# Kernel optimization log

Hardware: AMD Instinct MI355X
Metric: run time of the kernel (lower is better)

## Reference

```python
import jax, jax.numpy as jnp
import numpy as np

B, K, L, D, H = 8, 64, 4096, 1024, 16
HD = D // H
SCALE = HD ** -0.5


def setup_inputs() -> dict:
    key = jax.random.key(0)
    ks = jax.random.split(key, 7)
    return {
        "query": jax.random.normal(ks[0], (B, K, D), jnp.float32),
        "key": jax.random.normal(ks[1], (B, L, D), jnp.float32),
        "value": jax.random.normal(ks[2], (B, L, D), jnp.float32),
        "Wq": jax.random.normal(ks[3], (D, D), jnp.float32) * (D ** -0.5),
        "Wk": jax.random.normal(ks[4], (D, D), jnp.float32) * (D ** -0.5),
        "Wv": jax.random.normal(ks[5], (D, D), jnp.float32) * (D ** -0.5),
        "Wo": jax.random.normal(ks[6], (D, D), jnp.float32) * (D ** -0.5),
        "bo": jnp.zeros((D,), jnp.float32),
    }


def reference(query, key, value, Wq, Wk, Wv, Wo, bo):
    # torch Linear: y = x @ W.T; split heads -> [B,H,len,HD]
    q = jnp.einsum('bkd,ed->bke', query, Wq).reshape(B, K, H, HD).transpose(0, 2, 1, 3)
    k = jnp.einsum('bld,ed->ble', key, Wk).reshape(B, L, H, HD).transpose(0, 2, 1, 3)
    v = jnp.einsum('bld,ed->ble', value, Wv).reshape(B, L, H, HD).transpose(0, 2, 1, 3)
    dots = jnp.einsum('bhkc,bhlc->bhkl', q, k) * SCALE  # [B,H,K,L]
    attn = jax.nn.softmax(dots, axis=-2)               # softmax over query (slot) dim
    attn = attn / (attn.sum(axis=-1, keepdims=True) + 1e-8)  # renormalize over keys
    out = jnp.einsum('bhkl,bhlc->bhkc', attn, v)       # [B,H,K,HD]
    out = out.transpose(0, 2, 1, 3).reshape(B, K, D)
    out = jnp.einsum('bkd,ed->bke', out, Wo) + bo
    return out, attn
```

## Files before the change

### kernel.cpp

```cpp
#include <hip/hip_runtime.h>
#include <hip/hip_bf16.h>

#define B_   8
#define KS_  64
#define L_   4096
#define D_   1024
#define H_   16
#define HD_  64
#define SCALE_ 0.125f

typedef __attribute__((ext_vector_type(8))) short short8;
typedef __attribute__((ext_vector_type(8))) unsigned short ushort8;
typedef __attribute__((ext_vector_type(4))) unsigned short ushort4v;
typedef __attribute__((ext_vector_type(4))) float f32x4;

__device__ __forceinline__ unsigned short f2b(float f) {
  union { float f; unsigned u; } v; v.f = f;
  unsigned r = v.u + 0x7fffu + ((v.u >> 16) & 1u);
  return (unsigned short)(r >> 16);
}

typedef const __attribute__((address_space(1))) void gas_void;
typedef __attribute__((address_space(3))) void las_void;
__device__ __forceinline__ void gl2lds16(const void* g, void* l) {
  __builtin_amdgcn_global_load_lds((gas_void*)g, (las_void*)l, 16, 0, 0);
}

__global__ __launch_bounds__(256) void wcvt(const float* __restrict__ wq,
                                            const float* __restrict__ wk,
                                            const float* __restrict__ wv,
                                            const float* __restrict__ wo,
                                            unsigned short* __restrict__ out) {
  int i = blockIdx.x * 256 + threadIdx.x;
  int seg = i >> 18;
  int off = (i & 0x3ffff) << 2;
  const float* src = (seg == 0) ? wq : (seg == 1) ? wk : (seg == 2) ? wv : wo;
  f32x4 v = *(const f32x4*)(src + off);
  ushort4v o;
#pragma unroll
  for (int j = 0; j < 4; ++j) o[j] = f2b(v[j]);
  *(ushort4v*)(out + ((size_t)seg << 20) + off) = o;
}

__global__ __launch_bounds__(256) void cvt_qkv(const float* __restrict__ q,
                                               const float* __restrict__ k,
                                               const float* __restrict__ v,
                                               unsigned short* __restrict__ qb,
                                               unsigned short* __restrict__ kb,
                                               unsigned short* __restrict__ vb) {
  const int Q4 = 131072, K4 = 8388608;
  const int total = Q4 + 2 * K4;
  for (int i = blockIdx.x * 256 + threadIdx.x; i < total; i += gridDim.x * 256) {
    const float* src; unsigned short* dst; int off;
    if (i < Q4)            { src = q; dst = qb; off = i; }
    else if (i < Q4 + K4)  { src = k; dst = kb; off = i - Q4; }
    else                   { src = v; dst = vb; off = i - Q4 - K4; }
    f32x4 x = *(const f32x4*)(src + (size_t)off * 4);
    ushort4v o;
#pragma unroll
    for (int j = 0; j < 4; ++j) o[j] = f2b(x[j]);
    *(ushort4v*)(dst + (size_t)off * 4) = o;
  }
}

template <bool OUT_F32B>
__global__ __launch_bounds__(256) void gemm_bf16(const unsigned short* __restrict__ A,
                                                 const unsigned short* __restrict__ W,
                                                 void* __restrict__ Cp,
                                                 const float* __restrict__ bias) {
  __shared__ __align__(16) char smem[34816];
  const int tid = threadIdx.x, lane = tid & 63, wv = tid >> 6;
  const int g = lane >> 4, c15 = lane & 15;
  const int wm = wv >> 1, wn = wv & 1;

  const int nwg = gridDim.x;
  const int swz = (blockIdx.x & 7) * (nwg >> 3) + (blockIdx.x >> 3);
  const long m0 = (long)(swz >> 3) * 128;
  const int  n0 = (swz & 7) * 128;

  const int srow = lane >> 2, scol = (lane & 3) * 8;
  const unsigned short* a_src = A + (m0 + srow) * 1024 + scol;
  const unsigned short* b_src = W + (long)(n0 + srow) * 1024 + scol;

  f32x4 acc[4][4] = {};

  auto stage = [&](int buf, int kt) {
    unsigned short* al = (unsigned short*)(smem + buf * 8192);
    unsigned short* bl = (unsigned short*)(smem + 16384 + buf * 8192);
#pragma unroll
    for (int q = 0; q < 2; ++q) {
      const int rbase = q * 64 + wv * 16;
      gl2lds16(a_src + (long)rbase * 1024 + kt * 32, al + rbase * 32);
      gl2lds16(b_src + (long)rbase * 1024 + kt * 32, bl + rbase * 32);
    }
  };

  stage(0, 0);
  __syncthreads();

  int cur = 0;
  for (int kt = 0; kt < 32; ++kt) {
    if (kt + 1 < 32) stage(cur ^ 1, kt + 1);
    const unsigned short* al = (const unsigned short*)(smem + cur * 8192);
    const unsigned short* bl = (const unsigned short*)(smem + 16384 + cur * 8192);
    short8 af[4];
#pragma unroll
    for (int m = 0; m < 4; ++m)
      af[m] = *(const short8*)&al[(wm * 64 + m * 16 + c15) * 32 + g * 8];
#pragma unroll
    for (int n = 0; n < 4; ++n) {
      short8 b8 = *(const short8*)&bl[(wn * 64 + n * 16 + c15) * 32 + g * 8];
#pragma unroll
      for (int m = 0; m < 4; ++m)
        acc[m][n] = __builtin_amdgcn_mfma_f32_16x16x32_bf16(af[m], b8, acc[m][n], 0, 0, 0);
    }
    __syncthreads();
    cur ^= 1;
  }

  if constexpr (OUT_F32B) {
    float* Cf = (float*)Cp;
#pragma unroll
    for (int m = 0; m < 4; ++m)
#pragma unroll
      for (int n = 0; n < 4; ++n)
#pragma unroll
        for (int r = 0; r < 4; ++r) {
          long row = m0 + wm * 64 + m * 16 + g * 4 + r;
          int  col = n0 + wn * 64 + n * 16 + c15;
          Cf[row * 1024 + col] = acc[m][n][r] + bias[col];
        }
  } else {
    unsigned short* c_lds = (unsigned short*)smem;
#pragma unroll
    for (int m = 0; m < 4; ++m)
#pragma unroll
      for (int n = 0; n < 4; ++n)
#pragma unroll
        for (int r = 0; r < 4; ++r)
          c_lds[(wm * 64 + m * 16 + g * 4 + r) * 132 + wn * 64 + n * 16 + c15] =
              f2b(acc[m][n][r]);
    __syncthreads();
    unsigned short* Cb = (unsigned short*)Cp;
    const int row = tid >> 1, half = tid & 1;
    unsigned short*       dst = Cb + (m0 + row) * 1024 + n0 + half * 64;
    const unsigned short* sl  = &c_lds[row * 132 + half * 64];
#pragma unroll
    for (int i = 0; i < 8; ++i)
      *(ushort8*)(dst + i * 8) = *(const ushort8*)(sl + i * 8);
  }
}

__global__ __launch_bounds__(512) void attn_pass1(const unsigned short* __restrict__ q_b,
                                                  const unsigned short* __restrict__ k_b,
                                                  float* __restrict__ rs_part) {
  __shared__ unsigned short q_lds[64][72];
  __shared__ unsigned short k_lds[128][72];
  __shared__ float rs_lds[8][64];
  const int bh = blockIdx.x >> 2, ch = blockIdx.x & 3;
  const int b = bh >> 4, h = bh & 15;
  const int tid = threadIdx.x;
  const int w = tid >> 6, lane = tid & 63;
  const int g = lane >> 4, c15 = lane & 15;

  {
    int slot = tid >> 3, cc = (tid & 7) * 8;
    *(ushort8*)&q_lds[slot][cc] =
        *(const ushort8*)(q_b + (long)(b * 64 + slot) * 1024 + h * 64 + cc);
  }

  float rs[4][4] = {};
  const long kbase = (long)b * L_ * D_ + h * 64;
  const int  sl = tid >> 2, sc = (tid & 3) * 16;

  for (int it = ch * 8; it < ch * 8 + 8; ++it) {
    const int l0 = it * 128;
    ushort8 k0 = *(const ushort8*)(k_b + kbase + (long)(l0 + sl) * 1024 + sc);
    ushort8 k1 = *(const ushort8*)(k_b + kbase + (long)(l0 + sl) * 1024 + sc + 8);
    __syncthreads();
    *(ushort8*)&k_lds[sl][sc]     = k0;
    *(ushort8*)&k_lds[sl][sc + 8] = k1;
    __syncthreads();

    f32x4 s[4] = {};
#pragma unroll
    for (int ks = 0; ks < 2; ++ks) {
      short8 bf = *(const short8*)&k_lds[w * 16 + c15][ks * 32 + g * 8];
#pragma unroll
      for (int m = 0; m < 4; ++m) {
        short8 af = *(const short8*)&q_lds[m * 16 + c15][ks * 32 + g * 8];
        s[m] = __builtin_amdgcn_mfma_f32_16x16x32_bf16(af, bf, s[m], 0, 0, 0);
      }
    }
    float mx = -1e30f;
#pragma unroll
    for (int m = 0; m < 4; ++m)
#pragma unroll
      for (int r = 0; r < 4; ++r) mx = fmaxf(mx, s[m][r]);
    mx = fmaxf(mx, __shfl_xor(mx, 16));
    mx = fmaxf(mx, __shfl_xor(mx, 32));
    float sum = 0.f, p[4][4];
#pragma unroll
    for (int m = 0; m < 4; ++m)
#pragma unroll
      for (int r = 0; r < 4; ++r) { p[m][r] = __expf((s[m][r] - mx) * SCALE_); sum += p[m][r]; }
    sum += __shfl_xor(sum, 16);
    sum += __shfl_xor(sum, 32);
    float rinv = 1.0f / sum;
#pragma unroll
    for (int m = 0; m < 4; ++m)
#pragma unroll
      for (int r = 0; r < 4; ++r) rs[m][r] += p[m][r] * rinv;
  }
#pragma unroll
  for (int m = 0; m < 4; ++m)
#pragma unroll
    for (int r = 0; r < 4; ++r) {
      float v = rs[m][r];
      v += __shfl_xor(v, 1); v += __shfl_xor(v, 2);
      v += __shfl_xor(v, 4); v += __shfl_xor(v, 8);
      if (c15 == 0) rs_lds[w][m * 16 + g * 4 + r] = v;
    }
  __syncthreads();
  if (tid < 64) {
    float t = 0.f;
#pragma unroll
    for (int w2 = 0; w2 < 8; ++w2) t += rs_lds[w2][tid];
    rs_part[(bh * 4 + ch) * 64 + tid] = t;
  }
}

__global__ __launch_bounds__(512) void attn_pass2(const unsigned short* __restrict__ q_b,
                                                  const unsigned short* __restrict__ k_b,
                                                  const unsigned short* __restrict__ v_b,
                                                  const float* __restrict__ rs_part,
                                                  float* __restrict__ attn,
                                                  float* __restrict__ op_part) {
  __shared__ unsigned short q_lds[64][72];
  __shared__ unsigned short k_lds[128][72];
  __shared__ unsigned short vt_lds[64][136];
  __shared__ unsigned short pt_lds[64][136];
  const int bh = blockIdx.x >> 2, ch = blockIdx.x & 3;
  const int b = bh >> 4, h = bh & 15;
  const int tid = threadIdx.x;
  const int w = tid >> 6, lane = tid & 63;
  const int g = lane >> 4, c15 = lane & 15;

  {
    int slot = tid >> 3, cc = (tid & 7) * 8;
    *(ushort8*)&q_lds[slot][cc] =
        *(const ushort8*)(q_b + (long)(b * 64 + slot) * 1024 + h * 64 + cc);
  }

  float inv_r[4][4];
#pragma unroll
  for (int m = 0; m < 4; ++m)
#pragma unroll
    for (int r = 0; r < 4; ++r) {
      int slot = m * 16 + g * 4 + r;
      float s = 0.f;
#pragma unroll
      for (int c = 0; c < 4; ++c) s += rs_part[(bh * 4 + c) * 64 + slot];
      inv_r[m][r] = 1.0f / (s + 1e-8f);
    }

  f32x4 oacc[2] = {};
  const int m_pv = w >> 1, n_pv0 = (w & 1) * 2;
  float* attn_base = attn + (long)bh * KS_ * L_;
  const long base_bld = (long)b * L_ * D_ + h * 64;
  const int  sl = tid >> 2, sc = (tid & 3) * 16;

  for (int it = ch * 8; it < ch * 8 + 8; ++it) {
    const int l0 = it * 128;
    ushort8 k0 = *(const ushort8*)(k_b + base_bld + (long)(l0 + sl) * 1024 + sc);
    ushort8 k1 = *(const ushort8*)(k_b + base_bld + (long)(l0 + sl) * 1024 + sc + 8);
    ushort8 v0 = *(const ushort8*)(v_b + base_bld + (long)(l0 + sl) * 1024 + sc);
    ushort8 v1 = *(const ushort8*)(v_b + base_bld + (long)(l0 + sl) * 1024 + sc + 8);
    __syncthreads();
    *(ushort8*)&k_lds[sl][sc]     = k0;
    *(ushort8*)&k_lds[sl][sc + 8] = k1;
#pragma unroll
    for (int j = 0; j < 8; ++j) {
      vt_lds[sc + j][sl]     = v0[j];
      vt_lds[sc + 8 + j][sl] = v1[j];
    }
    __syncthreads();

    f32x4 s[4] = {};
#pragma unroll
    for (int ks = 0; ks < 2; ++ks) {
      short8 bf = *(const short8*)&k_lds[w * 16 + c15][ks * 32 + g * 8];
#pragma unroll
      for (int m = 0; m < 4; ++m) {
        short8 af = *(const short8*)&q_lds[m * 16 + c15][ks * 32 + g * 8];
        s[m] = __builtin_amdgcn_mfma_f32_16x16x32_bf16(af, bf, s[m], 0, 0, 0);
      }
    }
    float mx = -1e30f;
#pragma unroll
    for (int m = 0; m < 4; ++m)
#pragma unroll
      for (int r = 0; r < 4; ++r) mx = fmaxf(mx, s[m][r]);
    mx = fmaxf(mx, __shfl_xor(mx, 16));
    mx = fmaxf(mx, __shfl_xor(mx, 32));
    float sum = 0.f, p[4][4];
#pragma unroll
    for (int m = 0; m < 4; ++m)
#pragma unroll
      for (int r = 0; r < 4; ++r) { p[m][r] = __expf((s[m][r] - mx) * SCALE_); sum += p[m][r]; }
    sum += __shfl_xor(sum, 16);
    sum += __shfl_xor(sum, 32);
    float rinv = 1.0f / sum;

    const int lloc = w * 16 + c15;
#pragma unroll
    for (int m = 0; m < 4; ++m)
#pragma unroll
      for (int r = 0; r < 4; ++r) {
        float ps = p[m][r] * rinv * inv_r[m][r];
        attn_base[(long)(m * 16 + g * 4 + r) * L_ + l0 + lloc] = ps;
        pt_lds[m * 16 + g * 4 + r][lloc] = f2b(ps);
      }
    __syncthreads();

#pragma unroll
    for (int ks = 0; ks < 4; ++ks) {
      short8 pa = *(const short8*)&pt_lds[m_pv * 16 + c15][ks * 32 + g * 8];
#pragma unroll
      for (int n2 = 0; n2 < 2; ++n2) {
        short8 vb = *(const short8*)&vt_lds[(n_pv0 + n2) * 16 + c15][ks * 32 + g * 8];
        oacc[n2] = __builtin_amdgcn_mfma_f32_16x16x32_bf16(pa, vb, oacc[n2], 0, 0, 0);
      }
    }
  }

#pragma unroll
  for (int n2 = 0; n2 < 2; ++n2)
#pragma unroll
    for (int r = 0; r < 4; ++r) {
      int slot = m_pv * 16 + g * 4 + r;
      int c    = (n_pv0 + n2) * 16 + c15;
      op_part[((long)(bh * 4 + ch) * 64 + slot) * 64 + c] = oacc[n2][r];
    }
}

__global__ __launch_bounds__(256) void oh_red(const float* __restrict__ op_part,
                                              unsigned short* __restrict__ oh) {
  int i = blockIdx.x * 256 + threadIdx.x;
  int c = i & 63, slot = (i >> 6) & 63, bh = i >> 12;
  float s = 0.f;
#pragma unroll
  for (int ch = 0; ch < 4; ++ch)
    s += op_part[((long)(bh * 4 + ch) * 64 + slot) * 64 + c];
  int b = bh >> 4, h = bh & 15;
  oh[(long)(b * 64 + slot) * 1024 + h * 64 + c] = f2b(s);
}

extern "C" void kernel_launch(void* const* d_in, const int* in_sizes, int n_in,
                              void* d_out, int out_size, void* d_ws, size_t ws_size,
                              hipStream_t stream) {
  (void)in_sizes; (void)n_in; (void)out_size; (void)ws_size;
  const float* query = (const float*)d_in[0];
  const float* key   = (const float*)d_in[1];
  const float* value = (const float*)d_in[2];
  const float* Wq    = (const float*)d_in[3];
  const float* Wk    = (const float*)d_in[4];
  const float* Wv    = (const float*)d_in[5];
  const float* Wo    = (const float*)d_in[6];
  const float* bo    = (const float*)d_in[7];

  char* ws = (char*)d_ws;
  unsigned short* w_all   = (unsigned short*)ws;
  unsigned short* wq_b    = w_all;
  unsigned short* wk_b    = w_all + (1u << 20);
  unsigned short* wv_b    = w_all + (2u << 20);
  unsigned short* wo_b    = w_all + (3u << 20);
  unsigned short* qin_b   = (unsigned short*)(ws + ((size_t)8  << 20));
  unsigned short* q_b     = (unsigned short*)(ws + ((size_t)9  << 20));
  unsigned short* oh_b    = (unsigned short*)(ws + ((size_t)10 << 20));
  float*          rs_part = (float*)         (ws + ((size_t)11 << 20));
  float*          op_part = (float*)         (ws + ((size_t)12 << 20));
  unsigned short* k_b     = (unsigned short*)(ws + ((size_t)20 << 20));
  unsigned short* v_b     = (unsigned short*)(ws + ((size_t)84 << 20));

  float* out  = (float*)d_out;
  float* attn = out + (size_t)B_ * KS_ * D_;

  unsigned short* kin_b = (unsigned short*)attn;
  unsigned short* vin_b = (unsigned short*)attn + ((size_t)32 << 20);

  wcvt<<<4096, 256, 0, stream>>>(Wq, Wk, Wv, Wo, w_all);
  cvt_qkv<<<2048, 256, 0, stream>>>(query, key, value, qin_b, kin_b, vin_b);

  gemm_bf16<false><<<32,   256, 0, stream>>>(qin_b, wq_b, q_b, nullptr);
  gemm_bf16<false><<<2048, 256, 0, stream>>>(kin_b, wk_b, k_b, nullptr);
  gemm_bf16<false><<<2048, 256, 0, stream>>>(vin_b, wv_b, v_b, nullptr);

  attn_pass1<<<512, 512, 0, stream>>>(q_b, k_b, rs_part);
  attn_pass2<<<512, 512, 0, stream>>>(q_b, k_b, v_b, rs_part, attn, op_part);
  oh_red<<<2048, 256, 0, stream>>>(op_part, oh_b);

  gemm_bf16<true><<<32, 256, 0, stream>>>(oh_b, wo_b, out, bo);
}
```

Measured before the change: 420.9 us.

## Add 256x256-tile double-buffered bf16 GEMM for K and V projections

Adds a new 512-thread GEMM kernel with 256x256 output tiles, 128KB LDS double buffering via direct global-to-LDS loads, XOR-swizzled LDS layout, and interleaved stage/MFMA phases with priority boosts. It replaces the 128x128 gemm for the large K and V projections (32768x1024x1024 each). Larger tiles raise arithmetic intensity and cut global reloads. The cost is lower occupancy and a fragile hand-written waitcnt/barrier schedule.

New measurement: 391.5 us. 1.08x faster.

```diff
diff --git a/kernel.cpp b/kernel.cpp
--- a/kernel.cpp
+++ b/kernel.cpp
@@ -24,6 +24,15 @@
 typedef __attribute__((address_space(3))) void las_void;
 __device__ __forceinline__ void gl2lds16(const void* g, void* l) {
   __builtin_amdgcn_global_load_lds((gas_void*)g, (las_void*)l, 16, 0, 0);
+}
+
+__device__ __forceinline__ void bar() {
+  asm volatile("" ::: "memory");
+  __builtin_amdgcn_s_barrier();
+  asm volatile("" ::: "memory");
+}
+__device__ __forceinline__ void vm4() {
+  asm volatile("s_waitcnt vmcnt(4)" ::: "memory");
 }
 
 __global__ __launch_bounds__(256) void wcvt(const float* __restrict__ wq,
@@ -63,6 +72,97 @@
   }
 }
 
+__global__ __launch_bounds__(512, 2) void gemm256(const unsigned short* __restrict__ A,
+                                                  const unsigned short* __restrict__ W,
+                                                  unsigned short* __restrict__ C) {
+  __shared__ __align__(16) char smem[131072];
+  const int tid = threadIdx.x, lane = tid & 63, w = tid >> 6;
+  const int g = lane >> 4, c15 = lane & 15;
+  const int wm = w >> 2, wn = w & 3;
+
+  const int swz = (blockIdx.x & 7) * 64 + (blockIdx.x >> 3);
+  const long m0 = (long)(swz >> 2) * 256;
+  const int  n0 = (swz & 2 * 2 - 1) * 256;
+
+  const int srow = w * 16 + (lane >> 2);
+  const int cswz = (lane & 3) ^ ((lane >> 2) & 3);
+  const unsigned short* a_sr = A + (m0 + srow) * 1024 + cswz * 8;
+  const unsigned short* b_sr = W + (long)(n0 + srow) * 1024 + cswz * 8;
+  const int rswz = (g ^ (c15 & 3)) << 4;
+  const int aoff = (wm * 128 + c15) * 64 + rswz;
+  const int boff = 65536 + (wn * 64 + c15) * 64 + rswz;
+
+  f32x4 acc[8][4] = {};
+  short8 af[8], bf[2];
+
+  auto STAGE_A = [&](int d, int kh, int tk) {
+    char* dst = smem + d * 32768 + kh * 16384 + w * 1024;
+    const unsigned short* src = a_sr + tk * 64 + kh * 32;
+    gl2lds16(src,          dst);
+    gl2lds16(src + 131072, dst + 8192);
+  };
+  auto STAGE_B = [&](int d, int kh, int tk) {
+    char* dst = smem + 65536 + d * 32768 + kh * 16384 + w * 1024;
+    const unsigned short* src = b_sr + tk * 64 + kh * 32;
+    gl2lds16(src,          dst);
+    gl2lds16(src + 131072, dst + 8192);
+  };
+  auto LDA = [&](int d, int ks) {
+    const char* base = smem + d * 32768 + ks * 16384 + aoff;
+#pragma unroll
+    for (int m = 0; m < 8; ++m) af[m] = *(const short8*)(base + m * 1024);
+  };
+  auto LDB = [&](int d, int ks, int nh) {
+    const char* base = smem + d * 32768 + ks * 16384 + boff + nh * 2048;
+    bf[0] = *(const short8*)(base);
+    bf[1] = *(const short8*)(base + 1024);
+  };
+  auto MM = [&](int nh) {
+    __builtin_amdgcn_s_setprio(1);
+#pragma unroll
+    for (int n2 = 0; n2 < 2; ++n2)
+#pragma unroll
+      for (int m = 0; m < 8; ++m)
+        acc[m][nh * 2 + n2] =
+            __builtin_amdgcn_mfma_f32_16x16x32_bf16(af[m], bf[n2], acc[m][nh * 2 + n2], 0, 0, 0);
+    __builtin_amdgcn_s_setprio(0);
+  };
+
+  STAGE_A(0, 0, 0); STAGE_B(0, 0, 0); STAGE_A(0, 1, 0); STAGE_B(0, 1, 0);
+  vm4();
+  bar();
+
+#pragma unroll 1
+  for (int tk = 0; tk < 16; tk += 2) {
+    const bool more = (tk + 2 < 16);
+    LDA(0, 0); LDB(0, 0, 0); STAGE_A(1, 0, tk + 1);          bar(); MM(0); bar();
+    LDB(0, 0, 1);            STAGE_B(1, 0, tk + 1);  vm4();  bar(); MM(1); bar();
+    LDA(0, 1); LDB(0, 1, 0); STAGE_A(1, 1, tk + 1);          bar(); MM(0); bar();
+    LDB(0, 1, 1);            STAGE_B(1, 1, tk + 1);  vm4();  bar(); MM(1); bar();
+    LDA(1, 0); LDB(1, 0, 0); if (more) STAGE_A(0, 0, tk + 2);        bar(); MM(0); bar();
+    LDB(1, 0, 1);            if (more) STAGE_B(0, 0, tk + 2); vm4(); bar(); MM(1); bar();
+    LDA(1, 1); LDB(1, 1, 0); if (more) STAGE_A(0, 1, tk + 2);        bar(); MM(0); bar();
+    LDB(1, 1, 1);            if (more) STAGE_B(0, 1, tk + 2); vm4(); bar(); MM(1); bar();
+  }
+
+  unsigned short* cl = (unsigned short*)smem;
+#pragma unroll
+  for (int m = 0; m < 8; ++m)
+#pragma unroll
+    for (int n = 0; n < 4; ++n)
+#pragma unroll
+      for (int r = 0; r < 4; ++r)
+        cl[(wm * 128 + m * 16 + g * 4 + r) * 256 + wn * 64 + n * 16 + c15] =
+            f2b(acc[m][n][r]);
+  __syncthreads();
+  const int row = tid >> 1, half = tid & 1;
+  unsigned short*       dst = C + (m0 + row) * 1024 + n0 + half * 128;
+  const unsigned short* sl  = cl + row * 256 + half * 128;
+#pragma unroll
+  for (int i = 0; i < 16; ++i)
+    *(ushort8*)(dst + i * 8) = *(const ushort8*)(sl + i * 8);
+}
+
 template <bool OUT_F32B>
 __global__ __launch_bounds__(256) void gemm_bf16(const unsigned short* __restrict__ A,
                                                  const unsigned short* __restrict__ W,
@@ -392,9 +492,9 @@
   wcvt<<<4096, 256, 0, stream>>>(Wq, Wk, Wv, Wo, w_all);
   cvt_qkv<<<2048, 256, 0, stream>>>(query, key, value, qin_b, kin_b, vin_b);
 
-  gemm_bf16<false><<<32,   256, 0, stream>>>(qin_b, wq_b, q_b, nullptr);
-  gemm_bf16<false><<<2048, 256, 0, stream>>>(kin_b, wk_b, k_b, nullptr);
-  gemm_bf16<false><<<2048, 256, 0, stream>>>(vin_b, wv_b, v_b, nullptr);
+  gemm_bf16<false><<<32, 256, 0, stream>>>(qin_b, wq_b, q_b, nullptr);
+  gemm256<<<512, 512, 0, stream>>>(kin_b, wk_b, k_b);
+  gemm256<<<512, 512, 0, stream>>>(vin_b, wv_b, v_b);
 
   attn_pass1<<<512, 512, 0, stream>>>(q_b, k_b, rs_part);
   attn_pass2<<<512, 512, 0, stream>>>(q_b, k_b, v_b, rs_part, attn, op_part);
```
